# Optimization experiments

Measured on AMD Instinct MI355X. Metric: run time of the kernel, lower is better.

## Reference

```python
import jax, jax.numpy as jnp
import numpy as np

N_QUBITS = 9   # kernelsize**2
N_LAYERS = 2   # BasicEntanglerLayers depth
KS = 3
FILTERS = 4


def _rx(theta):
    # RX(theta) = [[cos(t/2), -i sin(t/2)], [-i sin(t/2), cos(t/2)]]
    c = jnp.cos(theta / 2).astype(jnp.complex64)
    s = (-1j) * jnp.sin(theta / 2).astype(jnp.complex64)
    return jnp.stack([jnp.stack([c, s]), jnp.stack([s, c])])


def _apply_1q(state, gate, wire):
    # state: (2,)*N_QUBITS complex64
    s = jnp.moveaxis(state, wire, 0).reshape(2, -1)
    s = gate @ s
    return jnp.moveaxis(s.reshape((2,) * N_QUBITS), 0, wire)


def _apply_cnot(state, c, t):
    s0 = jnp.take(state, 0, axis=c)
    s1 = jnp.take(state, 1, axis=c)
    ft = t if t < c else t - 1  # target axis index after removing control axis
    s1 = jnp.flip(s1, axis=ft)
    return jnp.stack([s0, s1], axis=c)


def _circuit(p, w):
    # p: (N_QUBITS,) input angles; w: (N_LAYERS, N_QUBITS) trainable angles
    state = jnp.zeros((2,) * N_QUBITS, dtype=jnp.complex64).at[(0,) * N_QUBITS].set(1.0)
    # AngleEmbedding (rotation='X', PennyLane default)
    for i in range(N_QUBITS):
        state = _apply_1q(state, _rx(p[i]), i)
    # BasicEntanglerLayers: RX rotations + CNOT ring per layer
    for l in range(N_LAYERS):
        for i in range(N_QUBITS):
            state = _apply_1q(state, _rx(w[l, i]), i)
        for i in range(N_QUBITS):
            state = _apply_cnot(state, i, (i + 1) % N_QUBITS)
    probs = state.real ** 2 + state.imag ** 2
    z = []
    for i in range(N_QUBITS):
        pi = probs.sum(axis=tuple(a for a in range(N_QUBITS) if a != i))  # (2,)
        z.append(pi[0] - pi[1])  # <Z_i>
    return jnp.stack(z)  # (N_QUBITS,)


def setup_inputs() -> dict:
    key = jax.random.key(0)
    k1, k2 = jax.random.split(key)
    x = jax.random.normal(k1, (4, 3, 28, 28), dtype=jnp.float32)
    qweights = jax.random.uniform(k2, (N_LAYERS, N_QUBITS), dtype=jnp.float32, minval=0.0, maxval=2.0 * np.pi)
    return {"x": x, "qweights": qweights}


def reference(x, qweights):
    B, C, H, W = x.shape
    h_out = H - KS + 1
    w_out = W - KS + 1
    # Patch extraction: (B, C, h_out, w_out, KS*KS)
    patches = jnp.stack(
        [x[:, :, dy:dy + h_out, dx:dx + w_out] for dy in range(KS) for dx in range(KS)],
        axis=-1,
    )
    # With stride=1 the overlapping scatter writes in the original are fully
    # overwritten by later iterations, so out[b,f,y,x,c] == circuit(patch)[f].
    q = jax.vmap(_circuit, in_axes=(0, None))(patches.reshape(-1, KS * KS), qweights)
    q = q.reshape(B, C, h_out, w_out, N_QUBITS)[..., :FILTERS]
    out = q.mean(axis=1)  # mean over channels -> (B, h_out, w_out, F)
    return jnp.transpose(out, (0, 3, 1, 2))  # (B, F, h_out, w_out)
```

## Files before the change

kernel.cpp:

```cpp
#include <hip/hip_runtime.h>


static constexpr int BQ = 4;
static constexpr int CH = 3;
static constexpr int HOUT = 26;
static constexpr int WOUT = 26;

__device__ __forceinline__ float shflx(float v, int m) {
  return __shfl_xor(v, m, 64);
}

__global__ __launch_bounds__(192) void quanv_kernel(
    const float* __restrict__ x,
    const float* __restrict__ w,
    float* __restrict__ out)
{
  __shared__ float sm[CH * 4];

  const int pix  = blockIdx.x;
  const int b    = pix / (HOUT * WOUT);
  const int r    = pix % (HOUT * WOUT);
  const int oy   = r / WOUT;
  const int ox   = r % WOUT;
  const int ch   = threadIdx.x >> 6;
  const int lane = threadIdx.x & 63;

  float ci[9], si[9];
#pragma unroll
  for (int i = 0; i < 9; ++i) {
    const int dy = i / 3, dx = i % 3;
    const float p  = x[((b * CH + ch) * 28 + (oy + dy)) * 28 + (ox + dx)];
    const float th = 0.5f * (p + w[i]);
    ci[i] = __cosf(th);
    si[i] = __sinf(th);
  }
  float c1[9], s1[9];
#pragma unroll
  for (int q = 0; q < 9; ++q) {
    const float th = 0.5f * w[9 + q];
    c1[q] = __cosf(th);
    s1[q] = __sinf(th);
  }

  float plo = 1.f;
#pragma unroll
  for (int q = 0; q < 6; ++q)
    plo *= ((lane >> q) & 1) ? si[q] : ci[q];
  const int pclo = __popc(lane);

  float tr[8], ti[8];
#pragma unroll
  for (int k = 0; k < 8; ++k) {
    const float r8 = plo * ((k & 1) ? si[6] : ci[6])
                         * ((k & 2) ? si[7] : ci[7])
                         * ((k & 4) ? si[8] : ci[8]);
    const int pc = (pclo + __popc(k)) & 3;
    tr[k] = (pc == 0) ? r8 : ((pc == 2) ? -r8 : 0.f);
    ti[k] = (pc == 3) ? r8 : ((pc == 1) ? -r8 : 0.f);
  }

  constexpr int LXm[9] = {3, 6, 12, 24, 48, 32, 0, 0, 3};
  constexpr int KXm[9] = {0, 0, 0,  0,  0,  1,  3, 6, 4};
#pragma unroll
  for (int q = 0; q < 9; ++q) {
    const float c = c1[q], s = s1[q];
    float pr[8], pim[8];
#pragma unroll
    for (int k = 0; k < 8; ++k) {
      float vr = tr[k ^ KXm[q]];
      float vi = ti[k ^ KXm[q]];
      if (LXm[q] != 0) {
        vr = shflx(vr, LXm[q]);
        vi = shflx(vi, LXm[q]);
      }
      pr[k] = vr;
      pim[k] = vi;
    }
#pragma unroll
    for (int k = 0; k < 8; ++k) {
      const float ntr = c * tr[k] + s * pim[k];
      const float nti = c * ti[k] - s * pr[k];
      tr[k] = ntr;
      ti[k] = nti;
    }
  }

  float prob[8];
#pragma unroll
  for (int k = 0; k < 8; ++k) prob[k] = tr[k] * tr[k] + ti[k] * ti[k];

  constexpr int ROW[4] = {0x154, 0x1FD, 0x1FA, 0x1F5};
  float z[4];
#pragma unroll
  for (int f = 0; f < 4; ++f) {
    const int hi = ROW[f] >> 6;
    const int lo = ROW[f] & 63;
    float acc = 0.f;
#pragma unroll
    for (int k = 0; k < 8; ++k)
      acc += (__popc(hi & k) & 1) ? -prob[k] : prob[k];
    z[f] = (__popc(lo & lane) & 1) ? -acc : acc;
  }

#pragma unroll
  for (int m = 1; m < 64; m <<= 1) {
#pragma unroll
    for (int f = 0; f < 4; ++f) z[f] += shflx(z[f], m);
  }
  if (lane == 0) {
#pragma unroll
    for (int f = 0; f < 4; ++f) sm[ch * 4 + f] = z[f];
  }
  __syncthreads();

  if (threadIdx.x < 4) {
    const int f = threadIdx.x;
    const float v = (sm[f] + sm[4 + f] + sm[8 + f]) * (1.f / 3.f);
    out[((b * 4 + f) * HOUT + oy) * WOUT + ox] = v;
  }
}

extern "C" void kernel_launch(void* const* d_in, const int* in_sizes, int n_in,
                              void* d_out, int out_size, void* d_ws, size_t ws_size,
                              hipStream_t stream) {
  const float* x = (const float*)d_in[0];
  const float* w = (const float*)d_in[1];
  float* out = (float*)d_out;
  dim3 grid(BQ * HOUT * WOUT);
  dim3 block(192);
  hipLaunchKernelGGL(quanv_kernel, grid, block, 0, stream, x, w, out);
}
```

Measured before the change: 69.16 us.

## Replace state-vector simulation with closed-form Pauli-Z expectation formulas

Drops the per-pixel 512-amplitude state-vector simulation (shuffles across a 64-lane wave per channel) and uses derived closed-form trigonometric polynomials for the four measured Z expectations. Each thread now handles one pixel and loops over the three channels, so the shared-memory reduction and block barrier go away. This removes most of the arithmetic and cross-lane traffic. The risk is that the hand-derived formulas are valid only for this fixed circuit (9 qubits, 2 layers, ring CNOT) and must be exactly right.

```diff
diff --git a/kernel.cpp b/kernel.cpp
--- a/kernel.cpp
+++ b/kernel.cpp
@@ -1,123 +1,86 @@
 #include <hip/hip_runtime.h>
 
 
-static constexpr int BQ = 4;
 static constexpr int CH = 3;
 static constexpr int HOUT = 26;
 static constexpr int WOUT = 26;
+static constexpr int NPIX = 4 * HOUT * WOUT;
 
-__device__ __forceinline__ float shflx(float v, int m) {
-  return __shfl_xor(v, m, 64);
-}
-
-__global__ __launch_bounds__(192) void quanv_kernel(
+__global__ __launch_bounds__(64) void quanv_closed(
     const float* __restrict__ x,
     const float* __restrict__ w,
     float* __restrict__ out)
 {
-  __shared__ float sm[CH * 4];
+  const int pix = blockIdx.x * 64 + threadIdx.x;
+  if (pix >= NPIX) return;
+  const int b  = pix / (HOUT * WOUT);
+  const int r  = pix % (HOUT * WOUT);
+  const int oy = r / WOUT;
+  const int ox = r % WOUT;
 
-  const int pix  = blockIdx.x;
-  const int b    = pix / (HOUT * WOUT);
-  const int r    = pix % (HOUT * WOUT);
-  const int oy   = r / WOUT;
-  const int ox   = r % WOUT;
-  const int ch   = threadIdx.x >> 6;
-  const int lane = threadIdx.x & 63;
+  float cw[9], sw[9];
+#pragma unroll
+  for (int q = 0; q < 9; ++q) __sincosf(w[9 + q], &sw[q], &cw[q]);
 
-  float ci[9], si[9];
+  const float CC01 = cw[0] * cw[1], SS01 = sw[0] * sw[1];
+  const float CC12 = cw[1] * cw[2], SS12 = sw[1] * sw[2];
+  const float CC23 = cw[2] * cw[3], SS23 = sw[2] * sw[3];
+  const float CC45 = cw[4] * cw[5], SS45 = sw[4] * sw[5];
+  const float CC67 = cw[6] * cw[7], SS67 = sw[6] * sw[7];
+  const float C18  = cw[1] * cw[8];
+
+  const float W000 =  C18 * CC23 * CC45 * CC67;
+  const float W100 =  C18 * SS23 * CC45 * CC67;
+  const float W010 =  C18 * CC23 * SS45 * CC67;
+  const float W001 =  C18 * CC23 * CC45 * SS67;
+  const float W110 = -C18 * SS23 * SS45 * CC67;
+  const float W101 =  C18 * SS23 * CC45 * SS67;
+  const float W011 = -C18 * CC23 * SS45 * SS67;
+  const float W111 =  C18 * SS23 * SS45 * SS67;
+
+  const float K2a = cw[0] * CC12, K2b = cw[0] * SS12;
+  const float K300 =  CC01 * CC23, K310 = SS01 * CC23;
+  const float K301 =  CC01 * SS23, K311 = -SS01 * SS23;
+
+  float acc0 = 0.f, acc1 = 0.f, acc2 = 0.f, acc3 = 0.f;
+
 #pragma unroll
-  for (int i = 0; i < 9; ++i) {
-    const int dy = i / 3, dx = i % 3;
-    const float p  = x[((b * CH + ch) * 28 + (oy + dy)) * 28 + (ox + dx)];
-    const float th = 0.5f * (p + w[i]);
-    ci[i] = __cosf(th);
-    si[i] = __sinf(th);
-  }
-  float c1[9], s1[9];
+  for (int ch = 0; ch < CH; ++ch) {
+    float cf[9], sf[9];
 #pragma unroll
-  for (int q = 0; q < 9; ++q) {
-    const float th = 0.5f * w[9 + q];
-    c1[q] = __cosf(th);
-    s1[q] = __sinf(th);
+    for (int i = 0; i < 9; ++i) {
+      const int dy = i / 3, dx = i % 3;
+      const float p = x[((b * CH + ch) * 28 + (oy + dy)) * 28 + (ox + dx)];
+      __sincosf(p + w[i], &sf[i], &cf[i]);
+    }
+
+    acc0 += W000 * cf[2] * cf[4] * cf[6] * cf[8]
+          + W100 * sf[2] * sf[4] * cf[6] * cf[8]
+          + W010 * cf[2] * sf[4] * sf[6] * cf[8]
+          + W001 * cf[2] * cf[4] * sf[6] * sf[8]
+          + W110 * sf[2] * cf[4] * sf[6] * cf[8]
+          + W101 * sf[2] * sf[4] * sf[6] * sf[8]
+          + W011 * cf[2] * sf[4] * cf[6] * sf[8]
+          + W111 * sf[2] * cf[4] * cf[6] * sf[8];
+
+    const float c5678  = cf[5] * cf[6] * cf[7] * cf[8];
+    const float c45678 = cf[4] * c5678;
+
+    acc1 += cf[3] * c45678 * (CC01 * cf[0] * cf[2] + SS01 * sf[0] * sf[2]);
+
+    acc2 += c45678 * (K2a * cf[1] * cf[3] + K2b * sf[1] * sf[3]);
+
+    acc3 += c5678 * (K300 * cf[0] * cf[2] * cf[4]
+                   + K310 * sf[0] * sf[2] * cf[4]
+                   + K301 * cf[0] * sf[2] * sf[4]
+                   + K311 * sf[0] * cf[2] * sf[4]);
   }
 
-  float plo = 1.f;
-#pragma unroll
-  for (int q = 0; q < 6; ++q)
-    plo *= ((lane >> q) & 1) ? si[q] : ci[q];
-  const int pclo = __popc(lane);
-
-  float tr[8], ti[8];
-#pragma unroll
-  for (int k = 0; k < 8; ++k) {
-    const float r8 = plo * ((k & 1) ? si[6] : ci[6])
-                         * ((k & 2) ? si[7] : ci[7])
-                         * ((k & 4) ? si[8] : ci[8]);
-    const int pc = (pclo + __popc(k)) & 3;
-    tr[k] = (pc == 0) ? r8 : ((pc == 2) ? -r8 : 0.f);
-    ti[k] = (pc == 3) ? r8 : ((pc == 1) ? -r8 : 0.f);
-  }
-
-  constexpr int LXm[9] = {3, 6, 12, 24, 48, 32, 0, 0, 3};
-  constexpr int KXm[9] = {0, 0, 0,  0,  0,  1,  3, 6, 4};
-#pragma unroll
-  for (int q = 0; q < 9; ++q) {
-    const float c = c1[q], s = s1[q];
-    float pr[8], pim[8];
-#pragma unroll
-    for (int k = 0; k < 8; ++k) {
-      float vr = tr[k ^ KXm[q]];
-      float vi = ti[k ^ KXm[q]];
-      if (LXm[q] != 0) {
-        vr = shflx(vr, LXm[q]);
-        vi = shflx(vi, LXm[q]);
-      }
-      pr[k] = vr;
-      pim[k] = vi;
-    }
-#pragma unroll
-    for (int k = 0; k < 8; ++k) {
-      const float ntr = c * tr[k] + s * pim[k];
-      const float nti = c * ti[k] - s * pr[k];
-      tr[k] = ntr;
-      ti[k] = nti;
-    }
-  }
-
-  float prob[8];
-#pragma unroll
-  for (int k = 0; k < 8; ++k) prob[k] = tr[k] * tr[k] + ti[k] * ti[k];
-
-  constexpr int ROW[4] = {0x154, 0x1FD, 0x1FA, 0x1F5};
-  float z[4];
-#pragma unroll
-  for (int f = 0; f < 4; ++f) {
-    const int hi = ROW[f] >> 6;
-    const int lo = ROW[f] & 63;
-    float acc = 0.f;
-#pragma unroll
-    for (int k = 0; k < 8; ++k)
-      acc += (__popc(hi & k) & 1) ? -prob[k] : prob[k];
-    z[f] = (__popc(lo & lane) & 1) ? -acc : acc;
-  }
-
-#pragma unroll
-  for (int m = 1; m < 64; m <<= 1) {
-#pragma unroll
-    for (int f = 0; f < 4; ++f) z[f] += shflx(z[f], m);
-  }
-  if (lane == 0) {
-#pragma unroll
-    for (int f = 0; f < 4; ++f) sm[ch * 4 + f] = z[f];
-  }
-  __syncthreads();
-
-  if (threadIdx.x < 4) {
-    const int f = threadIdx.x;
-    const float v = (sm[f] + sm[4 + f] + sm[8 + f]) * (1.f / 3.f);
-    out[((b * 4 + f) * HOUT + oy) * WOUT + ox] = v;
-  }
+  const float inv3 = 1.f / 3.f;
+  out[((b * 4 + 0) * HOUT + oy) * WOUT + ox] = acc0 * inv3;
+  out[((b * 4 + 1) * HOUT + oy) * WOUT + ox] = acc1 * inv3;
+  out[((b * 4 + 2) * HOUT + oy) * WOUT + ox] = acc2 * inv3;
+  out[((b * 4 + 3) * HOUT + oy) * WOUT + ox] = acc3 * inv3;
 }
 
 extern "C" void kernel_launch(void* const* d_in, const int* in_sizes, int n_in,
@@ -126,7 +89,7 @@
   const float* x = (const float*)d_in[0];
   const float* w = (const float*)d_in[1];
   float* out = (float*)d_out;
-  dim3 grid(BQ * HOUT * WOUT);
-  dim3 block(192);
-  hipLaunchKernelGGL(quanv_kernel, grid, block, 0, stream, x, w, out);
+  dim3 grid((NPIX + 63) / 64);
+  dim3 block(64);
+  hipLaunchKernelGGL(quanv_closed, grid, block, 0, stream, x, w, out);
 }
```

Measured after the change: 56.11 us. 1.23x faster.
